# Kernel tuning notes

Measured on AMD Instinct MI355X. Metric: run time of the kernel, lower is better.

The kernel has to match this reference:

```python
import jax, jax.numpy as jnp
import numpy as np

STRIDE = 1
PAD = 3
DIL = 1


def setup_inputs() -> dict:
    key = jax.random.key(0)
    k1, k2, k3 = jax.random.split(key, 3)
    B, C, H, W = 8, 256, 64, 64
    G, K = 4, 7
    Ho, Wo = 64, 64  # same-padding, stride 1
    return {
        "input": jax.random.normal(k1, (B, C, H, W), dtype=jnp.float32),
        "weight": jax.random.normal(k2, (B, G, K, K, Ho, Wo), dtype=jnp.float32),
        "bias": jax.random.normal(k3, (C,), dtype=jnp.float32),
    }


def reference(input, weight, bias):
    # input: [B,C,H,W], weight: [B,G,Kh,Kw,Ho,Wo], bias: [C]
    B, C, H, W = input.shape
    G, Kh, Kw, Ho, Wo = weight.shape[1:]
    Cpg = C // G
    xp = jnp.pad(input, ((0, 0), (0, 0), (PAD, PAD), (PAD, PAD)))
    # group view: [B, G, C/G, H+2p, W+2p]
    xg = xp.reshape(B, G, Cpg, H + 2 * PAD, W + 2 * PAD)
    out = jnp.zeros((B, G, Cpg, Ho, Wo), dtype=input.dtype)
    # fused accumulation over the K*K kernel taps; no im2col blowup
    for kh in range(Kh):
        for kw in range(Kw):
            h0 = kh * DIL
            w0 = kw * DIL
            patch = xg[:, :, :, h0:h0 + Ho * STRIDE:STRIDE, w0:w0 + Wo * STRIDE:STRIDE]
            out = out + patch * weight[:, :, kh, kw][:, :, None, :, :]
    out = out.reshape(B, C, Ho, Wo) + bias[None, :, None, None]
    return out
```

## Files before the change

kernel.cpp:

```cpp
#include <hip/hip_runtime.h>


#define BLK_X 16
#define BLK_Y 16
#define NTHR  256
#define NC    4
#define ROWS  16
#define S_ROWS 22
#define S_STRIDE 72
#define S_CH (S_ROWS * S_STRIDE)
#define S_ELEMS (S_ROWS * 70)

__global__ __launch_bounds__(NTHR, 4)
void involution_kernel(const float* __restrict__ in,
                       const float* __restrict__ w,
                       const float* __restrict__ bias,
                       float* __restrict__ out) {
    __shared__ float lds[NC * S_CH];

    const int tx  = threadIdx.x;
    const int ty  = threadIdx.y;
    const int tid = ty * BLK_X + tx;
    const int x0  = tx * 4;
    const int Y0  = blockIdx.x * ROWS;
    const int y   = Y0 + ty;
    const int c0  = blockIdx.y * NC;
    const int bz  = blockIdx.z;
    const int g   = bz & 3;

    const float* inb  = in  + (size_t)bz * 64 * 4096;
    float*       outb = out + (size_t)bz * 64 * 4096;
    const float* wb   = w   + (size_t)bz * 49 * 4096 + y * 64 + x0;

    #pragma unroll
    for (int c = 0; c < NC; ++c) {
        const float* p = inb + (size_t)(c0 + c) * 4096;
        float* l = lds + c * S_CH;
        #pragma unroll
        for (int j = 0; j < 7; ++j) {
            int i = tid + j * NTHR;
            if (i < S_ELEMS) {
                int r  = i / 70;
                int cl = i - r * 70;
                int gy = Y0 + r - 3;
                int gx = cl - 3;
                float v = 0.f;
                if (gy >= 0 && gy < 64 && gx >= 0 && gx < 64)
                    v = p[gy * 64 + gx];
                l[r * S_STRIDE + cl] = v;
            }
        }
    }
    __syncthreads();

    float acc[NC][4];
    #pragma unroll
    for (int c = 0; c < NC; ++c) {
        acc[c][0] = 0.f; acc[c][1] = 0.f; acc[c][2] = 0.f; acc[c][3] = 0.f;
    }

    #pragma unroll 1
    for (int kh = 0; kh < 7; ++kh) {
        float4 wv[7];
        #pragma unroll
        for (int kw = 0; kw < 7; ++kw)
            wv[kw] = *(const float4*)(wb + (size_t)(kh * 7 + kw) * 4096);

        #pragma unroll
        for (int c = 0; c < NC; ++c) {
            const float* lr = lds + c * S_CH + (ty + kh) * S_STRIDE + x0;
            float4 va = *(const float4*)(lr);
            float4 vb = *(const float4*)(lr + 4);
            float2 vc = *(const float2*)(lr + 8);
            float vals[10] = {va.x, va.y, va.z, va.w,
                              vb.x, vb.y, vb.z, vb.w,
                              vc.x, vc.y};
            #pragma unroll
            for (int kw = 0; kw < 7; ++kw) {
                acc[c][0] += vals[kw + 0] * wv[kw].x;
                acc[c][1] += vals[kw + 1] * wv[kw].y;
                acc[c][2] += vals[kw + 2] * wv[kw].z;
                acc[c][3] += vals[kw + 3] * wv[kw].w;
            }
        }
    }

    #pragma unroll
    for (int c = 0; c < NC; ++c) {
        const float bv = bias[g * 64 + c0 + c];
        float4 o;
        o.x = acc[c][0] + bv;
        o.y = acc[c][1] + bv;
        o.z = acc[c][2] + bv;
        o.w = acc[c][3] + bv;
        *(float4*)(outb + (size_t)(c0 + c) * 4096 + y * 64 + x0) = o;
    }
}

extern "C" void kernel_launch(void* const* d_in, const int* in_sizes, int n_in,
                              void* d_out, int out_size, void* d_ws, size_t ws_size,
                              hipStream_t stream) {
    const float* in   = (const float*)d_in[0];
    const float* wgt  = (const float*)d_in[1];
    const float* bias = (const float*)d_in[2];
    float* out = (float*)d_out;

    dim3 block(BLK_X, BLK_Y, 1);
    dim3 grid(64 / ROWS, 64 / NC, 32);
    involution_kernel<<<grid, block, 0, stream>>>(in, wgt, bias, out);
}
```

Baseline: 140.8 us.

## Compute two output rows per thread and vectorize halo tile loads

Each thread now computes two adjacent output rows, so every LDS row read is shared across both rows' kernel taps: 8 row loads per channel instead of 14. The block shrinks to 128 threads with a waves-per-EU hint. The input halo fill now uses float4 segments with a one-float4 left pad instead of scalar per-element loads with divides. The cost is more registers (two weight sets and eight accumulators per channel) and possibly lower occupancy.

```diff
diff --git a/kernel.cpp b/kernel.cpp
--- a/kernel.cpp
+++ b/kernel.cpp
@@ -2,16 +2,18 @@
 
 
 #define BLK_X 16
-#define BLK_Y 16
-#define NTHR  256
+#define BLK_Y 8
+#define NTHR  128
 #define NC    4
-#define ROWS  16
+#define R     2
+#define TROWS (BLK_Y * R)
 #define S_ROWS 22
 #define S_STRIDE 72
 #define S_CH (S_ROWS * S_STRIDE)
-#define S_ELEMS (S_ROWS * 70)
+#define SEGS_PER_CH (S_ROWS * 18)
 
-__global__ __launch_bounds__(NTHR, 4)
+__global__ __launch_bounds__(NTHR)
+__attribute__((amdgpu_waves_per_eu(3)))
 void involution_kernel(const float* __restrict__ in,
                        const float* __restrict__ w,
                        const float* __restrict__ bias,
@@ -22,65 +24,83 @@
     const int ty  = threadIdx.y;
     const int tid = ty * BLK_X + tx;
     const int x0  = tx * 4;
-    const int Y0  = blockIdx.x * ROWS;
-    const int y   = Y0 + ty;
+    const int Y0  = blockIdx.x * TROWS;
     const int c0  = blockIdx.y * NC;
     const int bz  = blockIdx.z;
     const int g   = bz & 3;
 
     const float* inb  = in  + (size_t)bz * 64 * 4096;
     float*       outb = out + (size_t)bz * 64 * 4096;
-    const float* wb   = w   + (size_t)bz * 49 * 4096 + y * 64 + x0;
 
     #pragma unroll
-    for (int c = 0; c < NC; ++c) {
-        const float* p = inb + (size_t)(c0 + c) * 4096;
-        float* l = lds + c * S_CH;
+    for (int ch = 0; ch < NC; ++ch) {
+        const float* p = inb + (size_t)(c0 + ch) * 4096;
+        float* l = lds + ch * S_CH;
         #pragma unroll
-        for (int j = 0; j < 7; ++j) {
-            int i = tid + j * NTHR;
-            if (i < S_ELEMS) {
-                int r  = i / 70;
-                int cl = i - r * 70;
-                int gy = Y0 + r - 3;
-                int gx = cl - 3;
-                float v = 0.f;
-                if (gy >= 0 && gy < 64 && gx >= 0 && gx < 64)
-                    v = p[gy * 64 + gx];
-                l[r * S_STRIDE + cl] = v;
+        for (int j = 0; j < 4; ++j) {
+            int e = tid + j * NTHR;
+            if (e < SEGS_PER_CH) {
+                int row = e / 18;
+                int t   = e - row * 18;
+                int gy  = Y0 + row - 3;
+                float4 v = make_float4(0.f, 0.f, 0.f, 0.f);
+                if (t >= 1 && t <= 16 && gy >= 0 && gy < 64)
+                    v = *(const float4*)(p + gy * 64 + (t - 1) * 4);
+                *(float4*)(l + row * S_STRIDE + t * 4) = v;
             }
         }
     }
     __syncthreads();
 
-    float acc[NC][4];
+    float acc[NC][R][4];
     #pragma unroll
-    for (int c = 0; c < NC; ++c) {
-        acc[c][0] = 0.f; acc[c][1] = 0.f; acc[c][2] = 0.f; acc[c][3] = 0.f;
-    }
+    for (int c = 0; c < NC; ++c)
+        #pragma unroll
+        for (int r = 0; r < R; ++r)
+            #pragma unroll
+            for (int i = 0; i < 4; ++i) acc[c][r][i] = 0.f;
 
-    #pragma unroll 1
-    for (int kh = 0; kh < 7; ++kh) {
-        float4 wv[7];
-        #pragma unroll
-        for (int kw = 0; kw < 7; ++kw)
-            wv[kw] = *(const float4*)(wb + (size_t)(kh * 7 + kw) * 4096);
+    const float* wb = w + (size_t)bz * 49 * 4096 + (Y0 + ty * R) * 64 + x0;
 
+    #pragma unroll
+    for (int s = 0; s < 8; ++s) {
+        float4 wv0[7], wv1[7];
+        if (s <= 6) {
+            #pragma unroll
+            for (int kw = 0; kw < 7; ++kw)
+                wv0[kw] = *(const float4*)(wb + (size_t)(s * 7 + kw) * 4096);
+        }
+        if (s >= 1) {
+            #pragma unroll
+            for (int kw = 0; kw < 7; ++kw)
+                wv1[kw] = *(const float4*)(wb + (size_t)((s - 1) * 7 + kw) * 4096 + 64);
+        }
         #pragma unroll
         for (int c = 0; c < NC; ++c) {
-            const float* lr = lds + c * S_CH + (ty + kh) * S_STRIDE + x0;
+            const float* lr = lds + c * S_CH + (ty * R + s) * S_STRIDE + x0;
             float4 va = *(const float4*)(lr);
             float4 vb = *(const float4*)(lr + 4);
-            float2 vc = *(const float2*)(lr + 8);
-            float vals[10] = {va.x, va.y, va.z, va.w,
+            float4 vc = *(const float4*)(lr + 8);
+            float vals[12] = {va.x, va.y, va.z, va.w,
                               vb.x, vb.y, vb.z, vb.w,
-                              vc.x, vc.y};
-            #pragma unroll
-            for (int kw = 0; kw < 7; ++kw) {
-                acc[c][0] += vals[kw + 0] * wv[kw].x;
-                acc[c][1] += vals[kw + 1] * wv[kw].y;
-                acc[c][2] += vals[kw + 2] * wv[kw].z;
-                acc[c][3] += vals[kw + 3] * wv[kw].w;
+                              vc.x, vc.y, vc.z, vc.w};
+            if (s <= 6) {
+                #pragma unroll
+                for (int kw = 0; kw < 7; ++kw) {
+                    acc[c][0][0] += vals[kw + 1] * wv0[kw].x;
+                    acc[c][0][1] += vals[kw + 2] * wv0[kw].y;
+                    acc[c][0][2] += vals[kw + 3] * wv0[kw].z;
+                    acc[c][0][3] += vals[kw + 4] * wv0[kw].w;
+                }
+            }
+            if (s >= 1) {
+                #pragma unroll
+                for (int kw = 0; kw < 7; ++kw) {
+                    acc[c][1][0] += vals[kw + 1] * wv1[kw].x;
+                    acc[c][1][1] += vals[kw + 2] * wv1[kw].y;
+                    acc[c][1][2] += vals[kw + 3] * wv1[kw].z;
+                    acc[c][1][3] += vals[kw + 4] * wv1[kw].w;
+                }
             }
         }
     }
@@ -88,12 +108,16 @@
     #pragma unroll
     for (int c = 0; c < NC; ++c) {
         const float bv = bias[g * 64 + c0 + c];
-        float4 o;
-        o.x = acc[c][0] + bv;
-        o.y = acc[c][1] + bv;
-        o.z = acc[c][2] + bv;
-        o.w = acc[c][3] + bv;
-        *(float4*)(outb + (size_t)(c0 + c) * 4096 + y * 64 + x0) = o;
+        #pragma unroll
+        for (int r = 0; r < R; ++r) {
+            float4 o;
+            o.x = acc[c][r][0] + bv;
+            o.y = acc[c][r][1] + bv;
+            o.z = acc[c][r][2] + bv;
+            o.w = acc[c][r][3] + bv;
+            *(float4*)(outb + (size_t)(c0 + c) * 4096
+                       + (Y0 + ty * R + r) * 64 + x0) = o;
+        }
     }
 }
 
@@ -106,6 +130,6 @@
     float* out = (float*)d_out;
 
     dim3 block(BLK_X, BLK_Y, 1);
-    dim3 grid(64 / ROWS, 64 / NC, 32);
+    dim3 grid(64 / TROWS, 64 / NC, 32);
     involution_kernel<<<grid, block, 0, stream>>>(in, wgt, bias, out);
 }
```

Measured after the change: 209.5 us. 48.8% more time.

## Keep all 49 weight taps in registers and double-buffer channel tiles in LDS

Applied to the files above, without the earlier changes.

Each thread now loads its 49 per-pixel weight float4s into registers once and reuses them across 16 channels, where before it used 4. Input tiles are staged into a double-buffered LDS with float4 global loads, a 2-channel group at a time, so the next group's loads overlap compute on the current one. Block size drops to 128 threads with 8 rows, and waves_per_eu is pinned to 2 to allow a large register budget. The aims are to cut redundant weight traffic and to hide global load latency. In exchange the kernel uses very high register pressure and lower occupancy.

```diff
diff --git a/kernel.cpp b/kernel.cpp
--- a/kernel.cpp
+++ b/kernel.cpp
@@ -2,29 +2,63 @@
 
 
 #define BLK_X 16
-#define BLK_Y 16
-#define NTHR  256
-#define NC    4
-#define ROWS  16
-#define S_ROWS 22
+#define BLK_Y 8
+#define NTHR  128
+#define CH_PER_BLK 16
+#define NSTG 2
+#define NGRP (CH_PER_BLK / NSTG)
+#define S_ROWS 14
 #define S_STRIDE 72
 #define S_CH (S_ROWS * S_STRIDE)
-#define S_ELEMS (S_ROWS * 70)
+#define SEGS (S_ROWS * 18)
 
-__global__ __launch_bounds__(NTHR, 4)
+#define LOADG(dst, grp_) do {                                              \
+    _Pragma("unroll")                                                      \
+    for (int ch_ = 0; ch_ < NSTG; ++ch_) {                                 \
+        const float* p_ = inb + (size_t)(c0 + (grp_) * NSTG + ch_) * 4096; \
+        _Pragma("unroll")                                                  \
+        for (int j_ = 0; j_ < 2; ++j_) {                                   \
+            int e_ = tid + j_ * NTHR;                                      \
+            float4 v_ = make_float4(0.f, 0.f, 0.f, 0.f);                   \
+            if (e_ < SEGS) {                                               \
+                int row_ = e_ / 18;                                        \
+                int t_   = e_ - row_ * 18;                                 \
+                int gy_  = Y0 + row_ - 3;                                  \
+                if (t_ >= 1 && t_ <= 16 && gy_ >= 0 && gy_ < 64)           \
+                    v_ = *(const float4*)(p_ + gy_ * 64 + (t_ - 1) * 4);   \
+            }                                                              \
+            dst[ch_][j_] = v_;                                             \
+        }                                                                  \
+    }                                                                      \
+} while (0)
+
+#define WRITE_STAGE(bufp, src) do {                                        \
+    _Pragma("unroll")                                                      \
+    for (int ch_ = 0; ch_ < NSTG; ++ch_) {                                 \
+        _Pragma("unroll")                                                  \
+        for (int j_ = 0; j_ < 2; ++j_) {                                   \
+            int e_ = tid + j_ * NTHR;                                      \
+            if (e_ < SEGS)                                                 \
+                *(float4*)((bufp) + ch_ * S_CH + e_ * 4) = src[ch_][j_];   \
+        }                                                                  \
+    }                                                                      \
+} while (0)
+
+__global__ __launch_bounds__(NTHR)
+__attribute__((amdgpu_waves_per_eu(2, 2)))
 void involution_kernel(const float* __restrict__ in,
                        const float* __restrict__ w,
                        const float* __restrict__ bias,
                        float* __restrict__ out) {
-    __shared__ float lds[NC * S_CH];
+    __shared__ float lds[2][NSTG][S_CH];
 
     const int tx  = threadIdx.x;
     const int ty  = threadIdx.y;
     const int tid = ty * BLK_X + tx;
     const int x0  = tx * 4;
-    const int Y0  = blockIdx.x * ROWS;
+    const int Y0  = blockIdx.x * BLK_Y;
     const int y   = Y0 + ty;
-    const int c0  = blockIdx.y * NC;
+    const int c0  = blockIdx.y * CH_PER_BLK;
     const int bz  = blockIdx.z;
     const int g   = bz & 3;
 
@@ -32,68 +66,68 @@
     float*       outb = out + (size_t)bz * 64 * 4096;
     const float* wb   = w   + (size_t)bz * 49 * 4096 + y * 64 + x0;
 
+    float4 w4[49];
     #pragma unroll
-    for (int c = 0; c < NC; ++c) {
-        const float* p = inb + (size_t)(c0 + c) * 4096;
-        float* l = lds + c * S_CH;
-        #pragma unroll
-        for (int j = 0; j < 7; ++j) {
-            int i = tid + j * NTHR;
-            if (i < S_ELEMS) {
-                int r  = i / 70;
-                int cl = i - r * 70;
-                int gy = Y0 + r - 3;
-                int gx = cl - 3;
-                float v = 0.f;
-                if (gy >= 0 && gy < 64 && gx >= 0 && gx < 64)
-                    v = p[gy * 64 + gx];
-                l[r * S_STRIDE + cl] = v;
-            }
-        }
+    for (int k = 0; k < 49; ++k)
+        w4[k] = *(const float4*)(wb + (size_t)k * 4096);
+
+    float4 pf[NSTG][2];
+    LOADG(pf, 0);
+
+    float bvs[CH_PER_BLK];
+    #pragma unroll
+    for (int c = 0; c < CH_PER_BLK; ++c)
+        bvs[c] = bias[g * 64 + c0 + c];
+
+    #pragma unroll
+    for (int k = 0; k < 49; ++k) {
+        asm volatile("" : "+v"(w4[k].x), "+v"(w4[k].y),
+                          "+v"(w4[k].z), "+v"(w4[k].w));
     }
+
+    WRITE_STAGE(&lds[0][0][0], pf);
     __syncthreads();
 
-    float acc[NC][4];
-    #pragma unroll
-    for (int c = 0; c < NC; ++c) {
-        acc[c][0] = 0.f; acc[c][1] = 0.f; acc[c][2] = 0.f; acc[c][3] = 0.f;
-    }
+    #pragma unroll 1
+    for (int grp = 0; grp < NGRP; ++grp) {
+        float* cur = &lds[grp & 1][0][0];
+        float* nxt = &lds[(grp + 1) & 1][0][0];
+        const bool more = (grp + 1 < NGRP);
 
-    #pragma unroll 1
-    for (int kh = 0; kh < 7; ++kh) {
-        float4 wv[7];
-        #pragma unroll
-        for (int kw = 0; kw < 7; ++kw)
-            wv[kw] = *(const float4*)(wb + (size_t)(kh * 7 + kw) * 4096);
+        if (more) LOADG(pf, grp + 1);
 
         #pragma unroll
-        for (int c = 0; c < NC; ++c) {
-            const float* lr = lds + c * S_CH + (ty + kh) * S_STRIDE + x0;
-            float4 va = *(const float4*)(lr);
-            float4 vb = *(const float4*)(lr + 4);
-            float2 vc = *(const float2*)(lr + 8);
-            float vals[10] = {va.x, va.y, va.z, va.w,
-                              vb.x, vb.y, vb.z, vb.w,
-                              vc.x, vc.y};
+        for (int ch = 0; ch < NSTG; ++ch) {
+            const int c = grp * NSTG + ch;
+            float a0 = 0.f, a1 = 0.f, a2 = 0.f, a3 = 0.f;
             #pragma unroll
-            for (int kw = 0; kw < 7; ++kw) {
-                acc[c][0] += vals[kw + 0] * wv[kw].x;
-                acc[c][1] += vals[kw + 1] * wv[kw].y;
-                acc[c][2] += vals[kw + 2] * wv[kw].z;
-                acc[c][3] += vals[kw + 3] * wv[kw].w;
+            for (int kh = 0; kh < 7; ++kh) {
+                const float* lr = cur + ch * S_CH + (ty + kh) * S_STRIDE + x0;
+                float4 va = *(const float4*)(lr);
+                float4 vb = *(const float4*)(lr + 4);
+                float4 vc = *(const float4*)(lr + 8);
+                float vals[12] = {va.x, va.y, va.z, va.w,
+                                  vb.x, vb.y, vb.z, vb.w,
+                                  vc.x, vc.y, vc.z, vc.w};
+                #pragma unroll
+                for (int kw = 0; kw < 7; ++kw) {
+                    const float4 wv = w4[kh * 7 + kw];
+                    a0 += vals[kw + 1] * wv.x;
+                    a1 += vals[kw + 2] * wv.y;
+                    a2 += vals[kw + 3] * wv.z;
+                    a3 += vals[kw + 4] * wv.w;
+                }
             }
+            const float bv = bvs[c];
+            float4 o;
+            o.x = a0 + bv; o.y = a1 + bv; o.z = a2 + bv; o.w = a3 + bv;
+            *(float4*)(outb + (size_t)(c0 + c) * 4096 + y * 64 + x0) = o;
         }
-    }
 
-    #pragma unroll
-    for (int c = 0; c < NC; ++c) {
-        const float bv = bias[g * 64 + c0 + c];
-        float4 o;
-        o.x = acc[c][0] + bv;
-        o.y = acc[c][1] + bv;
-        o.z = acc[c][2] + bv;
-        o.w = acc[c][3] + bv;
-        *(float4*)(outb + (size_t)(c0 + c) * 4096 + y * 64 + x0) = o;
+        if (more) {
+            WRITE_STAGE(nxt, pf);
+            __syncthreads();
+        }
     }
 }
 
@@ -106,6 +140,6 @@
     float* out = (float*)d_out;
 
     dim3 block(BLK_X, BLK_Y, 1);
-    dim3 grid(64 / ROWS, 64 / NC, 32);
+    dim3 grid(64 / BLK_Y, 64 / CH_PER_BLK, 32);
     involution_kernel<<<grid, block, 0, stream>>>(in, wgt, bias, out);
 }
```

Result: slower. 346.4 us (+146.1%).

## Double-buffer weight loads across kernel rows and vectorize swizzled LDS tile

Applied to the files above, without the earlier changes.

Stages the input halo tile as float4 segments with an XOR swizzle instead of scalar loads with per-element division. Weight rows are double-buffered in registers so the next row's loads are issued while the current row is being accumulated, and the first loads overlap the tile fill. Bias loads are hoisted before the barrier. This raises register pressure (two sets of seven float4 weight buffers) under a four-blocks-per-SM launch bound, which could cause spills.

```diff
diff --git a/kernel.cpp b/kernel.cpp
--- a/kernel.cpp
+++ b/kernel.cpp
@@ -7,16 +7,44 @@
 #define NC    4
 #define ROWS  16
 #define S_ROWS 22
-#define S_STRIDE 72
-#define S_CH (S_ROWS * S_STRIDE)
-#define S_ELEMS (S_ROWS * 70)
+#define ST_F4 24
+#define S_CH_F4 (S_ROWS * ST_F4)
+#define SEGS (S_ROWS * 18)
+
+#define LOADW(buf, KH) do {                                                 \
+    _Pragma("unroll")                                                       \
+    for (int kw_ = 0; kw_ < 7; ++kw_)                                       \
+        buf[kw_] = *(const float4*)(wb + (size_t)((KH) * 7 + kw_) * 4096);  \
+} while (0)
+
+#define STEP(KH, W) do {                                                    \
+    const int row_ = ty + (KH);                       \
+    const int xm_  = row_ & 7;                                              \
+    _Pragma("unroll")                                                       \
+    for (int ch_ = 0; ch_ < NC; ++ch_) {                                    \
+        const float4* lp_ = lds4 + ch_ * S_CH_F4 + row_ * ST_F4;            \
+        float4 v0_ = lp_[(tx + 0) ^ xm_];                                   \
+        float4 v1_ = lp_[(tx + 1) ^ xm_];                                   \
+        float4 v2_ = lp_[(tx + 2) ^ xm_];                                   \
+        float vals_[12] = {v0_.x, v0_.y, v0_.z, v0_.w,                      \
+                           v1_.x, v1_.y, v1_.z, v1_.w,                      \
+                           v2_.x, v2_.y, v2_.z, v2_.w};                     \
+        _Pragma("unroll")                                                   \
+        for (int kw_ = 0; kw_ < 7; ++kw_) {                                 \
+            acc[ch_][0] += vals_[kw_ + 1] * W[kw_].x;                       \
+            acc[ch_][1] += vals_[kw_ + 2] * W[kw_].y;                       \
+            acc[ch_][2] += vals_[kw_ + 3] * W[kw_].z;                       \
+            acc[ch_][3] += vals_[kw_ + 4] * W[kw_].w;                       \
+        }                                                                   \
+    }                                                                       \
+} while (0)
 
 __global__ __launch_bounds__(NTHR, 4)
 void involution_kernel(const float* __restrict__ in,
                        const float* __restrict__ w,
                        const float* __restrict__ bias,
                        float* __restrict__ out) {
-    __shared__ float lds[NC * S_CH];
+    __shared__ float4 lds4[NC * S_CH_F4];
 
     const int tx  = threadIdx.x;
     const int ty  = threadIdx.y;
@@ -32,25 +60,32 @@
     float*       outb = out + (size_t)bz * 64 * 4096;
     const float* wb   = w   + (size_t)bz * 49 * 4096 + y * 64 + x0;
 
+    float4 wA[7], wB[7];
+    LOADW(wA, 0);
+
     #pragma unroll
-    for (int c = 0; c < NC; ++c) {
-        const float* p = inb + (size_t)(c0 + c) * 4096;
-        float* l = lds + c * S_CH;
+    for (int ch = 0; ch < NC; ++ch) {
+        const float* p = inb + (size_t)(c0 + ch) * 4096;
         #pragma unroll
-        for (int j = 0; j < 7; ++j) {
-            int i = tid + j * NTHR;
-            if (i < S_ELEMS) {
-                int r  = i / 70;
-                int cl = i - r * 70;
-                int gy = Y0 + r - 3;
-                int gx = cl - 3;
-                float v = 0.f;
-                if (gy >= 0 && gy < 64 && gx >= 0 && gx < 64)
-                    v = p[gy * 64 + gx];
-                l[r * S_STRIDE + cl] = v;
+        for (int j = 0; j < 2; ++j) {
+            int e = tid + j * NTHR;
+            if (e < SEGS) {
+                int row = e / 18;
+                int t   = e - row * 18;
+                int gy  = Y0 + row - 3;
+                float4 v = make_float4(0.f, 0.f, 0.f, 0.f);
+                if (t >= 1 && t <= 16 && gy >= 0 && gy < 64)
+                    v = *(const float4*)(p + gy * 64 + (t - 1) * 4);
+                lds4[ch * S_CH_F4 + row * ST_F4 + (t ^ (row & 7))] = v;
             }
         }
     }
+
+    float bvs[NC];
+    #pragma unroll
+    for (int c = 0; c < NC; ++c) bvs[c] = bias[g * 64 + c0 + c];
+
+    LOADW(wB, 1);
     __syncthreads();
 
     float acc[NC][4];
@@ -59,40 +94,21 @@
         acc[c][0] = 0.f; acc[c][1] = 0.f; acc[c][2] = 0.f; acc[c][3] = 0.f;
     }
 
-    #pragma unroll 1
-    for (int kh = 0; kh < 7; ++kh) {
-        float4 wv[7];
-        #pragma unroll
-        for (int kw = 0; kw < 7; ++kw)
-            wv[kw] = *(const float4*)(wb + (size_t)(kh * 7 + kw) * 4096);
-
-        #pragma unroll
-        for (int c = 0; c < NC; ++c) {
-            const float* lr = lds + c * S_CH + (ty + kh) * S_STRIDE + x0;
-            float4 va = *(const float4*)(lr);
-            float4 vb = *(const float4*)(lr + 4);
-            float2 vc = *(const float2*)(lr + 8);
-            float vals[10] = {va.x, va.y, va.z, va.w,
-                              vb.x, vb.y, vb.z, vb.w,
-                              vc.x, vc.y};
-            #pragma unroll
-            for (int kw = 0; kw < 7; ++kw) {
-                acc[c][0] += vals[kw + 0] * wv[kw].x;
-                acc[c][1] += vals[kw + 1] * wv[kw].y;
-                acc[c][2] += vals[kw + 2] * wv[kw].z;
-                acc[c][3] += vals[kw + 3] * wv[kw].w;
-            }
-        }
-    }
+    STEP(0, wA);  LOADW(wA, 2);
+    STEP(1, wB);  LOADW(wB, 3);
+    STEP(2, wA);  LOADW(wA, 4);
+    STEP(3, wB);  LOADW(wB, 5);
+    STEP(4, wA);  LOADW(wA, 6);
+    STEP(5, wB);
+    STEP(6, wA);
 
     #pragma unroll
     for (int c = 0; c < NC; ++c) {
-        const float bv = bias[g * 64 + c0 + c];
         float4 o;
-        o.x = acc[c][0] + bv;
-        o.y = acc[c][1] + bv;
-        o.z = acc[c][2] + bv;
-        o.w = acc[c][3] + bv;
+        o.x = acc[c][0] + bvs[c];
+        o.y = acc[c][1] + bvs[c];
+        o.z = acc[c][2] + bvs[c];
+        o.w = acc[c][3] + bvs[c];
         *(float4*)(outb + (size_t)(c0 + c) * 4096 + y * 64 + x0) = o;
     }
 }
```

New measurement: 125.3 us. 1.12x faster.
